# Kernel optimization log

Hardware: AMD Instinct MI355X
Metric: run time of the kernel (lower is better)

Reference implementation:

```python
import jax, jax.numpy as jnp
import numpy as np

T, B, D, H = 256, 128, 512, 512  # seq_len, batch, input_dim, hidden_dim (= n_qubits)


def setup_inputs() -> dict:
    key = jax.random.key(0)
    ks = jax.random.split(key, 17)
    s = 0.02
    inp = {"inputs": jax.random.normal(ks[0], (T, B, D), dtype=jnp.float32)}
    for j, n in enumerate(["f", "i", "u", "o"]):
        inp["W" + n] = jax.random.normal(ks[1 + 4 * j], (D + H, H), dtype=jnp.float32) * s
        inp["b" + n] = jnp.zeros((H,), jnp.float32)
        inp["rx" + n] = jax.random.normal(ks[2 + 4 * j], (H,), dtype=jnp.float32)
        inp["P" + n] = jax.random.normal(ks[3 + 4 * j], (H, H), dtype=jnp.float32) * s
    return inp


def _qlayer(z, rx, P):
    # per-wire trainable rotation RX(theta) acting on the scalar feature of each
    # wire (scales it by cos(theta)), followed by the bias-free `pre` linear.
    return (z * jnp.cos(rx)) @ P


def reference(inputs, Wf, bf, Wi, bi, Wu, bu, Wo, bo, rxf, rxi, rxu, rxo, Pf, Pi, Pu, Po):
    Bc, Hc = inputs.shape[1], bf.shape[0]

    def step(carry, x_t):
        hx, cx = carry
        comb = jnp.concatenate([x_t, hx], axis=1)  # (B, D+H)
        f = jax.nn.sigmoid(_qlayer(comb @ Wf + bf, rxf, Pf))
        i = jax.nn.sigmoid(_qlayer(comb @ Wi + bi, rxi, Pi))
        g = jnp.tanh(_qlayer(comb @ Wu + bu, rxu, Pu))
        o = jax.nn.sigmoid(_qlayer(comb @ Wo + bo, rxo, Po))
        cx = f * cx + i * g
        hx = o * jnp.tanh(cx)
        return (hx, cx), hx

    h0 = jnp.zeros((Bc, Hc), inputs.dtype)
    (hx, cx), outputs = jax.lax.scan(step, (h0, h0), inputs)
    return outputs, hx, cx
```

## Files before the change

### kernel.cpp

```cpp
#include <hip/hip_runtime.h>
#include <hip/hip_bf16.h>

typedef __attribute__((ext_vector_type(8))) short bf16x8;
typedef __attribute__((ext_vector_type(4))) float f32x4;
typedef unsigned short u16;
typedef unsigned int u32;

__device__ __forceinline__ u16 f2bf(float f) {
  union { float f; unsigned u; } v; v.f = f;
  unsigned r = v.u + 0x7FFFu + ((v.u >> 16) & 1u);
  return (u16)(r >> 16);
}

__device__ __forceinline__ float sigm_fast(float x) {
  return __builtin_amdgcn_rcpf(1.f + __expf(-x));
}
__device__ __forceinline__ float tanh_fast(float x) {
  x = fminf(fmaxf(x, -15.f), 15.f);
  float e = __expf(2.f * x);
  return (e - 1.f) * __builtin_amdgcn_rcpf(e + 1.f);
}

__device__ __forceinline__ void ld_llc_b128(const u16* p, bf16x8& r) {
  asm volatile("global_load_dwordx4 %0, %1, off sc0 sc1" : "=&v"(r) : "v"(p));
}
__device__ __forceinline__ void ld_g_b128(const u16* p, bf16x8& r) {
  asm volatile("global_load_dwordx4 %0, %1, off" : "=&v"(r) : "v"(p));
}
__device__ __forceinline__ void st_llc_b32(u32* p, u32 v) {
  asm volatile("global_store_dword %0, %1, off sc0 sc1" :: "v"(p), "v"(v) : "memory");
}
__device__ __forceinline__ void st_g_b32(u32* p, u32 v) {
  asm volatile("global_store_dword %0, %1, off" :: "v"(p), "v"(v) : "memory");
}

__global__ __launch_bounds__(256) void fold_kernel(
    const float* __restrict__ W0, const float* __restrict__ rx0, const float* __restrict__ P0,
    const float* __restrict__ W1, const float* __restrict__ rx1, const float* __restrict__ P1,
    const float* __restrict__ W2, const float* __restrict__ rx2, const float* __restrict__ P2,
    const float* __restrict__ W3, const float* __restrict__ rx3, const float* __restrict__ P3,
    u16* __restrict__ Wt)
{
  const int g = blockIdx.z;
  const float* W  = (g == 0) ? W0  : (g == 1) ? W1  : (g == 2) ? W2  : W3;
  const float* rx = (g == 0) ? rx0 : (g == 1) ? rx1 : (g == 2) ? rx2 : rx3;
  const float* P  = (g == 0) ? P0  : (g == 1) ? P1  : (g == 2) ? P2  : P3;
  __shared__ __align__(16) float As[16][68];
  __shared__ __align__(16) float Bs[16][68];
  const int bk = blockIdx.x, bj = blockIdx.y;
  const int tid = threadIdx.x;
  const int tx = tid & 15, ty = tid >> 4;
  const int j0 = bj * 64, k0 = bk * 64;
  float acc[4][4] = {};
  for (int m0 = 0; m0 < 512; m0 += 16) {
#pragma unroll
    for (int l = 0; l < 4; ++l) {
      int lin = tid + 256 * l;
      int mm = lin >> 6, jr = lin & 63;
      As[mm][jr] = P[(m0 + mm) * 512 + j0 + jr];
      int kk = lin >> 4, mb = lin & 15;
      Bs[mb][kk] = W[(k0 + kk) * 512 + m0 + mb] * cosf(rx[m0 + mb]);
    }
    __syncthreads();
#pragma unroll
    for (int mm = 0; mm < 16; ++mm) {
      f32x4 a = *(const f32x4*)&As[mm][ty * 4];
      f32x4 b = *(const f32x4*)&Bs[mm][tx * 4];
#pragma unroll
      for (int i = 0; i < 4; ++i)
#pragma unroll
        for (int jj = 0; jj < 4; ++jj)
          acc[i][jj] += a[i] * b[jj];
    }
    __syncthreads();
  }
#pragma unroll
  for (int i = 0; i < 4; ++i) {
    int j = j0 + ty * 4 + i;
    size_t n = (size_t)(j * 4 + g);
    ushort4 w;
    w.x = f2bf(acc[i][0]); w.y = f2bf(acc[i][1]);
    w.z = f2bf(acc[i][2]); w.w = f2bf(acc[i][3]);
    *(ushort4*)(Wt + n * 1024 + k0 + tx * 4) = w;
  }
}

__global__ __launch_bounds__(256) void fold_bias(
    const float* __restrict__ b0, const float* __restrict__ rx0, const float* __restrict__ P0,
    const float* __restrict__ b1, const float* __restrict__ rx1, const float* __restrict__ P1,
    const float* __restrict__ b2, const float* __restrict__ rx2, const float* __restrict__ P2,
    const float* __restrict__ b3, const float* __restrict__ rx3, const float* __restrict__ P3,
    float* __restrict__ bpn)
{
  const int g = blockIdx.x >> 3, jb = blockIdx.x & 7;
  const float* b  = (g == 0) ? b0  : (g == 1) ? b1  : (g == 2) ? b2  : b3;
  const float* rx = (g == 0) ? rx0 : (g == 1) ? rx1 : (g == 2) ? rx2 : rx3;
  const float* P  = (g == 0) ? P0  : (g == 1) ? P1  : (g == 2) ? P2  : P3;
  __shared__ float bc[512];
  __shared__ float red[4][65];
  const int tid = threadIdx.x;
  bc[tid] = b[tid] * cosf(rx[tid]);
  bc[tid + 256] = b[tid + 256] * cosf(rx[tid + 256]);
  __syncthreads();
  const int jl = tid & 63, msub = tid >> 6;
  const int j = jb * 64 + jl;
  float acc = 0.f;
  for (int m = msub * 128; m < msub * 128 + 128; ++m)
    acc += bc[m] * P[m * 512 + j];
  red[msub][jl] = acc;
  __syncthreads();
  if (msub == 0)
    bpn[j * 4 + g] = red[0][jl] + red[1][jl] + red[2][jl] + red[3][jl];
}

__global__ __launch_bounds__(256) void xcvt_kernel(
    const float* __restrict__ x, u16* __restrict__ xb)
{
  size_t i = (size_t)blockIdx.x * 256 + threadIdx.x;
  f32x4 v = *(const f32x4*)(x + i * 4);
  ushort4 w;
  w.x = f2bf(v[0]); w.y = f2bf(v[1]); w.z = f2bf(v[2]); w.w = f2bf(v[3]);
  *(ushort4*)(xb + i * 4) = w;
}

__global__ __launch_bounds__(256) void init_kernel(unsigned* hbuf32, float* cbuf,
                                                   unsigned* flags) {
  int i = blockIdx.x * 256 + threadIdx.x;
  hbuf32[i] = 0;
  cbuf[i] = 0.f;
  if (i < 256) flags[i] = 0;
}

__global__ __launch_bounds__(256) void tail_kernel(
    const float* __restrict__ hlast, const float* __restrict__ c,
    float* __restrict__ hx, float* __restrict__ cx)
{
  int i = blockIdx.x * 256 + threadIdx.x;
  hx[i] = hlast[i];
  cx[i] = c[i];
}

__global__ __launch_bounds__(256) void step_kernel(
    const u16* __restrict__ xb_t, const u16* __restrict__ h_in,
    u16* __restrict__ h_out, const u16* __restrict__ Wt,
    const float* __restrict__ bpn, float* __restrict__ cbuf,
    float* __restrict__ out_t)
{
  __shared__ float pre_s[32][33];
  const int bid = blockIdx.x;
  const int mb = bid >> 6, nb = bid & 63;
  const int b0 = mb * 32, n0 = nb * 32;
  const int tid = threadIdx.x;
  const int wv = tid >> 6, lane = tid & 63;
  const int rt = wv >> 1, nt = wv & 1;
  const int l15 = lane & 15, kg = lane >> 4;
  const int brow = b0 + rt * 16 + l15;
  const int ncol = n0 + nt * 16 + l15;
  const u16* wrow = Wt + (size_t)ncol * 1024;
  const u16* xrow = xb_t + (size_t)brow * 512;
  const u16* hrow = h_in + (size_t)brow * 512;
  f32x4 acc = {0.f, 0.f, 0.f, 0.f};
#pragma unroll 8
  for (int kk = 0; kk < 32; ++kk) {
    const int kb = kk * 32 + kg * 8;
    bf16x8 bfrag = *(const bf16x8*)(wrow + kb);
    bf16x8 afrag;
    if (kb < 512) afrag = *(const bf16x8*)(xrow + kb);
    else          afrag = *(const bf16x8*)(hrow + (kb - 512));
    acc = __builtin_amdgcn_mfma_f32_16x16x32_bf16(afrag, bfrag, acc, 0, 0, 0);
  }
  const float bias = bpn[ncol];
#pragma unroll
  for (int q = 0; q < 4; ++q)
    pre_s[rt * 16 + kg * 4 + q][nt * 16 + l15] = acc[q] + bias;
  __syncthreads();
  const int bb = tid >> 3, jo = tid & 7;
  float pf = pre_s[bb][jo * 4 + 0];
  float pi = pre_s[bb][jo * 4 + 1];
  float pu = pre_s[bb][jo * 4 + 2];
  float po = pre_s[bb][jo * 4 + 3];
  float fg = 1.f / (1.f + __expf(-pf));
  float ig = 1.f / (1.f + __expf(-pi));
  float gg = tanhf(pu);
  float og = 1.f / (1.f + __expf(-po));
  size_t idx = (size_t)(b0 + bb) * 512 + (size_t)(nb * 8 + jo);
  float cv = fg * cbuf[idx] + ig * gg;
  cbuf[idx] = cv;
  float hv = og * tanhf(cv);
  out_t[idx] = hv;
  h_out[idx] = f2bf(hv);
}

__global__ __launch_bounds__(256, 1) void qlstm_persistent(
    const u16* __restrict__ Xbf,
    u16* __restrict__ hbuf,
    const u16* __restrict__ Wt,
    const float* __restrict__ bpn,
    float* __restrict__ out,
    unsigned* __restrict__ flags)
{
  __shared__ float pre_s[32][33];
  const int bid = blockIdx.x;
  const int mb = bid >> 6, nb = bid & 63;
  const int b0 = mb * 32, n0 = nb * 32;
  const int tid = threadIdx.x;
  const int wv = tid >> 6, lane = tid & 63;
  const int rt = wv >> 1, nt = wv & 1;
  const int l15 = lane & 15, kg = lane >> 4;
  const int brow = b0 + rt * 16 + l15;
  const int ncol = n0 + nt * 16 + l15;

  const u16* wrow = Wt + (size_t)ncol * 1024;
  bf16x8 warr[32];
#pragma unroll
  for (int kk = 0; kk < 32; ++kk)
    warr[kk] = *(const bf16x8*)(wrow + kk * 32 + kg * 8);
  const float bnc = bpn[ncol];

  const int bb = tid >> 3, jo = tid & 7;
  const size_t eidx = (size_t)(b0 + bb) * 512 + (size_t)(nb * 8 + jo);
  float cst = 0.f, hl = 0.f;

  bf16x8 xf[16];
  {
    const u16* xr = Xbf + (size_t)brow * 512;
#pragma unroll
    for (int kk = 0; kk < 16; ++kk)
      ld_g_b128(xr + kk * 32 + kg * 8, xf[kk]);
    asm volatile("s_waitcnt vmcnt(0)" ::: "memory");
  }

  for (int t = 0; t < 256; ++t) {
    if (t > 0 && tid < 64) {
      int guard = 0;
      while (__hip_atomic_load(&flags[mb * 64 + tid], __ATOMIC_RELAXED,
                               __HIP_MEMORY_SCOPE_AGENT) < (unsigned)t) {
        __builtin_amdgcn_s_sleep(1);
        if (++guard > 8000) break;
      }
    }
    __builtin_amdgcn_s_barrier();
    asm volatile("" ::: "memory");

    bf16x8 hf[16];
    if (t > 0) {
      const u16* hr = hbuf + (size_t)((t & 1) ? 65536 : 0) + (size_t)brow * 512;
#pragma unroll
      for (int kk = 0; kk < 16; ++kk)
        ld_llc_b128(hr + kk * 32 + kg * 8, hf[kk]);
    }

    asm volatile("s_waitcnt vmcnt(16)" ::: "memory");
    __builtin_amdgcn_sched_barrier(0);
    f32x4 ax0 = {0,0,0,0}, ax1 = {0,0,0,0};
#pragma unroll
    for (int kk = 0; kk < 16; kk += 2) {
      ax0 = __builtin_amdgcn_mfma_f32_16x16x32_bf16(xf[kk],     warr[kk],     ax0, 0, 0, 0);
      ax1 = __builtin_amdgcn_mfma_f32_16x16x32_bf16(xf[kk + 1], warr[kk + 1], ax1, 0, 0, 0);
    }

    f32x4 ah0 = {0,0,0,0}, ah1 = {0,0,0,0};
    if (t > 0) {
      asm volatile("s_waitcnt vmcnt(0)" ::: "memory");
      __builtin_amdgcn_sched_barrier(0);
#pragma unroll
      for (int kk = 0; kk < 16; kk += 2) {
        ah0 = __builtin_amdgcn_mfma_f32_16x16x32_bf16(hf[kk],     warr[16 + kk],     ah0, 0, 0, 0);
        ah1 = __builtin_amdgcn_mfma_f32_16x16x32_bf16(hf[kk + 1], warr[16 + kk + 1], ah1, 0, 0, 0);
      }
    }
    f32x4 acc = (ax0 + ax1) + (ah0 + ah1);

#pragma unroll
    for (int q = 0; q < 4; ++q)
      pre_s[rt * 16 + kg * 4 + q][nt * 16 + l15] = acc[q] + bnc;
    asm volatile("s_waitcnt lgkmcnt(0)" ::: "memory");
    __builtin_amdgcn_sched_barrier(0);
    __builtin_amdgcn_s_barrier();
    asm volatile("" ::: "memory");

    float pf = pre_s[bb][jo * 4 + 0];
    float pi = pre_s[bb][jo * 4 + 1];
    float pu = pre_s[bb][jo * 4 + 2];
    float po = pre_s[bb][jo * 4 + 3];
    cst = sigm_fast(pf) * cst + sigm_fast(pi) * tanh_fast(pu);
    float hv = sigm_fast(po) * tanh_fast(cst);
    hl = hv;

    u16 myh = f2bf(hv);
    u32 partner = (u32)(u16)__shfl_xor((int)(u32)myh, 1);
    u16* hnext = hbuf + (size_t)(((t + 1) & 1) ? 65536 : 0);
    if ((tid & 1) == 0)
      st_llc_b32((u32*)(hnext + eidx), (u32)myh | (partner << 16));
    asm volatile("s_waitcnt vmcnt(0)" ::: "memory");
    __builtin_amdgcn_s_barrier();
    asm volatile("" ::: "memory");
    if (tid == 0)
      __hip_atomic_store(&flags[bid], (unsigned)(t + 1), __ATOMIC_RELAXED,
                         __HIP_MEMORY_SCOPE_AGENT);

    union { float f; u32 u; } ho; ho.f = hv;
    st_g_b32((u32*)(out + (size_t)t * 65536 + eidx), ho.u);
    if (t < 255) {
      const u16* xr = Xbf + (size_t)(t + 1) * 65536 + (size_t)brow * 512;
#pragma unroll
      for (int kk = 0; kk < 16; ++kk)
        ld_g_b128(xr + kk * 32 + kg * 8, xf[kk]);
    }
  }

  asm volatile("s_waitcnt vmcnt(0)" ::: "memory");
  out[(size_t)256 * 65536 + eidx] = hl;
  out[(size_t)256 * 65536 + 65536 + eidx] = cst;
}

extern "C" void kernel_launch(void* const* d_in, const int* in_sizes, int n_in,
                              void* d_out, int out_size, void* d_ws, size_t ws_size,
                              hipStream_t stream) {
  (void)in_sizes; (void)n_in; (void)out_size; (void)ws_size;
  const float* inp = (const float*)d_in[0];
  float* out = (float*)d_out;

  char* base = (char*)d_ws;
  u16*      Xbf   = (u16*)base;
  u16*      Wt    = (u16*)(base + 33554432);
  float*    bpn   = (float*)(base + 33554432 + 4194304);
  u16*      hbuf  = (u16*)(base + 33554432 + 4194304 + 8192);
  unsigned* flags = (unsigned*)(base + 33554432 + 4194304 + 8192 + 262144);
  float*    cbuf  = (float*)(base + 33554432 + 4194304 + 8192 + 262144 + 1024);

  const float* W[4];  const float* b[4];  const float* rx[4];  const float* P[4];
  for (int g = 0; g < 4; ++g) {
    W[g]  = (const float*)d_in[1 + 4 * g];
    b[g]  = (const float*)d_in[2 + 4 * g];
    rx[g] = (const float*)d_in[3 + 4 * g];
    P[g]  = (const float*)d_in[4 + 4 * g];
  }
  fold_kernel<<<dim3(16, 8, 4), 256, 0, stream>>>(
      W[0], rx[0], P[0], W[1], rx[1], P[1],
      W[2], rx[2], P[2], W[3], rx[3], P[3], Wt);
  fold_bias<<<dim3(32), 256, 0, stream>>>(
      b[0], rx[0], P[0], b[1], rx[1], P[1],
      b[2], rx[2], P[2], b[3], rx[3], P[3], bpn);
  xcvt_kernel<<<16384, 256, 0, stream>>>(inp, Xbf);
  init_kernel<<<256, 256, 0, stream>>>((unsigned*)hbuf, cbuf, flags);

  void* args[6];
  const u16* Xbf_c = Xbf;
  const u16* Wt_c = Wt;
  const float* bpn_c = bpn;
  u16* hbuf_p = hbuf;
  float* out_p = out;
  unsigned* flags_p = flags;
  args[0] = (void*)&Xbf_c;
  args[1] = (void*)&hbuf_p;
  args[2] = (void*)&Wt_c;
  args[3] = (void*)&bpn_c;
  args[4] = (void*)&out_p;
  args[5] = (void*)&flags_p;
  hipError_t e = hipLaunchCooperativeKernel((const void*)qlstm_persistent,
                                            dim3(256), dim3(256), args, 0, stream);
  if (e != hipSuccess) {
    for (int t = 0; t < 256; ++t) {
      const u16* xb_t  = Xbf + (size_t)t * 65536;
      const u16* h_in  = hbuf + (size_t)(t & 1) * 65536;
      u16*       h_oup = hbuf + (size_t)((t & 1) ^ 1) * 65536;
      float*     out_t = out + (size_t)t * 65536;
      step_kernel<<<256, 256, 0, stream>>>(xb_t, h_in, h_oup, Wt, bpn, cbuf, out_t);
    }
    tail_kernel<<<256, 256, 0, stream>>>(out + (size_t)255 * 65536, cbuf,
                                         out + (size_t)256 * 65536,
                                         out + (size_t)256 * 65536 + 65536);
  }
}
```

Baseline: 1.403 ms.

## Replace flag-based grid sync with sentinel-poisoned h slab polling

Removes the per-step flag array and block barrier wait, and instead makes consumers poll the h data itself. Slots in a 4-deep h ring are poisoned with a NaN sentinel pattern, and loads are retried until no sentinel remains. Each block re-poisons slot t+2 ahead of time. h stores are widened to 128-bit writes by shuffling four packed words into one lane, and pre_s is double-buffered so the trailing barrier can go. Block-to-tile mapping also changes so batch tiles interleave. The scheme relies on bf16 h never equalling the sentinel pair and on store ordering across the ring. It adds retry loads when data is not yet ready.

```diff
diff --git a/kernel.cpp b/kernel.cpp
--- a/kernel.cpp
+++ b/kernel.cpp
@@ -3,8 +3,11 @@
 
 typedef __attribute__((ext_vector_type(8))) short bf16x8;
 typedef __attribute__((ext_vector_type(4))) float f32x4;
+typedef __attribute__((ext_vector_type(4))) unsigned int u32x4;
 typedef unsigned short u16;
 typedef unsigned int u32;
+
+#define SENT 0x7FC07FC0u
 
 __device__ __forceinline__ u16 f2bf(float f) {
   union { float f; unsigned u; } v; v.f = f;
@@ -27,8 +30,8 @@
 __device__ __forceinline__ void ld_g_b128(const u16* p, bf16x8& r) {
   asm volatile("global_load_dwordx4 %0, %1, off" : "=&v"(r) : "v"(p));
 }
-__device__ __forceinline__ void st_llc_b32(u32* p, u32 v) {
-  asm volatile("global_store_dword %0, %1, off sc0 sc1" :: "v"(p), "v"(v) : "memory");
+__device__ __forceinline__ void st_llc_b128(u16* p, u32x4 v) {
+  asm volatile("global_store_dwordx4 %0, %1, off sc0 sc1" :: "v"(p), "v"(v) : "memory");
 }
 __device__ __forceinline__ void st_g_b32(u32* p, u32 v) {
   asm volatile("global_store_dword %0, %1, off" :: "v"(p), "v"(v) : "memory");
@@ -123,12 +126,13 @@
   *(ushort4*)(xb + i * 4) = w;
 }
 
-__global__ __launch_bounds__(256) void init_kernel(unsigned* hbuf32, float* cbuf,
-                                                   unsigned* flags) {
+__global__ __launch_bounds__(256) void init_kernel(u32* hslab32, u32* hz32,
+                                                   float* cbuf) {
   int i = blockIdx.x * 256 + threadIdx.x;
-  hbuf32[i] = 0;
+  hslab32[i] = SENT;
+  hslab32[i + 65536] = SENT;
+  hz32[i] = 0;
   cbuf[i] = 0.f;
-  if (i < 256) flags[i] = 0;
 }
 
 __global__ __launch_bounds__(256) void tail_kernel(
@@ -193,15 +197,14 @@
 
 __global__ __launch_bounds__(256, 1) void qlstm_persistent(
     const u16* __restrict__ Xbf,
-    u16* __restrict__ hbuf,
+    u16* __restrict__ hslab,
     const u16* __restrict__ Wt,
     const float* __restrict__ bpn,
-    float* __restrict__ out,
-    unsigned* __restrict__ flags)
-{
-  __shared__ float pre_s[32][33];
+    float* __restrict__ out)
+{
+  __shared__ float pre_s[2][32][33];
   const int bid = blockIdx.x;
-  const int mb = bid >> 6, nb = bid & 63;
+  const int mb = bid & 3, nb = bid >> 2;
   const int b0 = mb * 32, n0 = nb * 32;
   const int tid = threadIdx.x;
   const int wv = tid >> 6, lane = tid & 63;
@@ -219,6 +222,9 @@
 
   const int bb = tid >> 3, jo = tid & 7;
   const size_t eidx = (size_t)(b0 + bb) * 512 + (size_t)(nb * 8 + jo);
+  const bool pst = ((tid & 7) == 0);
+  const size_t prow_off = (size_t)(b0 + (tid >> 3)) * 512 + (size_t)(nb * 8);
+  const u32x4 sentv = {SENT, SENT, SENT, SENT};
   float cst = 0.f, hl = 0.f;
 
   bf16x8 xf[16];
@@ -231,27 +237,16 @@
   }
 
   for (int t = 0; t < 256; ++t) {
-    if (t > 0 && tid < 64) {
-      int guard = 0;
-      while (__hip_atomic_load(&flags[mb * 64 + tid], __ATOMIC_RELAXED,
-                               __HIP_MEMORY_SCOPE_AGENT) < (unsigned)t) {
-        __builtin_amdgcn_s_sleep(1);
-        if (++guard > 8000) break;
-      }
-    }
-    __builtin_amdgcn_s_barrier();
-    asm volatile("" ::: "memory");
-
+    const u16* hr = hslab + (size_t)(t & 3) * 65536 + (size_t)brow * 512;
     bf16x8 hf[16];
     if (t > 0) {
-      const u16* hr = hbuf + (size_t)((t & 1) ? 65536 : 0) + (size_t)brow * 512;
 #pragma unroll
       for (int kk = 0; kk < 16; ++kk)
         ld_llc_b128(hr + kk * 32 + kg * 8, hf[kk]);
     }
-
     asm volatile("s_waitcnt vmcnt(16)" ::: "memory");
     __builtin_amdgcn_sched_barrier(0);
+
     f32x4 ax0 = {0,0,0,0}, ax1 = {0,0,0,0};
 #pragma unroll
     for (int kk = 0; kk < 16; kk += 2) {
@@ -261,7 +256,24 @@
 
     f32x4 ah0 = {0,0,0,0}, ah1 = {0,0,0,0};
     if (t > 0) {
-      asm volatile("s_waitcnt vmcnt(0)" ::: "memory");
+      int guard = 0;
+      for (;;) {
+        asm volatile("s_waitcnt vmcnt(0)" ::: "memory");
+        __builtin_amdgcn_sched_barrier(0);
+        u32 bad = 0;
+#pragma unroll
+        for (int kk = 0; kk < 16; ++kk) {
+          union { bf16x8 v; u32 d[4]; } u; u.v = hf[kk];
+          bad |= (u.d[0] == SENT) | (u.d[1] == SENT)
+               | (u.d[2] == SENT) | (u.d[3] == SENT);
+        }
+        if (__all((int)(bad == 0))) break;
+        if (++guard > 30000) break;
+        __builtin_amdgcn_s_sleep(1);
+#pragma unroll
+        for (int kk = 0; kk < 16; ++kk)
+          ld_llc_b128(hr + kk * 32 + kg * 8, hf[kk]);
+      }
       __builtin_amdgcn_sched_barrier(0);
 #pragma unroll
       for (int kk = 0; kk < 16; kk += 2) {
@@ -271,34 +283,36 @@
     }
     f32x4 acc = (ax0 + ax1) + (ah0 + ah1);
 
+    if (pst)
+      st_llc_b128(hslab + (size_t)((t + 2) & 3) * 65536 + prow_off, sentv);
+
 #pragma unroll
     for (int q = 0; q < 4; ++q)
-      pre_s[rt * 16 + kg * 4 + q][nt * 16 + l15] = acc[q] + bnc;
+      pre_s[t & 1][rt * 16 + kg * 4 + q][nt * 16 + l15] = acc[q] + bnc;
     asm volatile("s_waitcnt lgkmcnt(0)" ::: "memory");
     __builtin_amdgcn_sched_barrier(0);
     __builtin_amdgcn_s_barrier();
     asm volatile("" ::: "memory");
 
-    float pf = pre_s[bb][jo * 4 + 0];
-    float pi = pre_s[bb][jo * 4 + 1];
-    float pu = pre_s[bb][jo * 4 + 2];
-    float po = pre_s[bb][jo * 4 + 3];
+    float pf = pre_s[t & 1][bb][jo * 4 + 0];
+    float pi = pre_s[t & 1][bb][jo * 4 + 1];
+    float pu = pre_s[t & 1][bb][jo * 4 + 2];
+    float po = pre_s[t & 1][bb][jo * 4 + 3];
     cst = sigm_fast(pf) * cst + sigm_fast(pi) * tanh_fast(pu);
     float hv = sigm_fast(po) * tanh_fast(cst);
     hl = hv;
 
     u16 myh = f2bf(hv);
-    u32 partner = (u32)(u16)__shfl_xor((int)(u32)myh, 1);
-    u16* hnext = hbuf + (size_t)(((t + 1) & 1) ? 65536 : 0);
-    if ((tid & 1) == 0)
-      st_llc_b32((u32*)(hnext + eidx), (u32)myh | (partner << 16));
+    u32 w  = (u32)myh | ((u32)(u16)__shfl_xor((int)(u32)myh, 1) << 16);
+    u32 d1 = (u32)__shfl_xor((int)w, 2);
+    u32 d2 = (u32)__shfl_xor((int)w, 4);
+    u32 d3 = (u32)__shfl_xor((int)w, 6);
+
     asm volatile("s_waitcnt vmcnt(0)" ::: "memory");
-    __builtin_amdgcn_s_barrier();
-    asm volatile("" ::: "memory");
-    if (tid == 0)
-      __hip_atomic_store(&flags[bid], (unsigned)(t + 1), __ATOMIC_RELAXED,
-                         __HIP_MEMORY_SCOPE_AGENT);
-
+    if (pst) {
+      u32x4 hw = {w, d1, d2, d3};
+      st_llc_b128(hslab + (size_t)((t + 1) & 3) * 65536 + prow_off, hw);
+    }
     union { float f; u32 u; } ho; ho.f = hv;
     st_g_b32((u32*)(out + (size_t)t * 65536 + eidx), ho.u);
     if (t < 255) {
@@ -322,12 +336,12 @@
   float* out = (float*)d_out;
 
   char* base = (char*)d_ws;
-  u16*      Xbf   = (u16*)base;
-  u16*      Wt    = (u16*)(base + 33554432);
-  float*    bpn   = (float*)(base + 33554432 + 4194304);
-  u16*      hbuf  = (u16*)(base + 33554432 + 4194304 + 8192);
-  unsigned* flags = (unsigned*)(base + 33554432 + 4194304 + 8192 + 262144);
-  float*    cbuf  = (float*)(base + 33554432 + 4194304 + 8192 + 262144 + 1024);
+  u16*   Xbf   = (u16*)base;
+  u16*   Wt    = (u16*)(base + 33554432);
+  float* bpn   = (float*)(base + 33554432 + 4194304);
+  u16*   hslab = (u16*)(base + 33554432 + 4194304 + 8192);
+  u16*   hz    = (u16*)(base + 33554432 + 4194304 + 8192 + 524288);
+  float* cbuf  = (float*)(base + 33554432 + 4194304 + 8192 + 524288 + 262144);
 
   const float* W[4];  const float* b[4];  const float* rx[4];  const float* P[4];
   for (int g = 0; g < 4; ++g) {
@@ -343,28 +357,26 @@
       b[0], rx[0], P[0], b[1], rx[1], P[1],
       b[2], rx[2], P[2], b[3], rx[3], P[3], bpn);
   xcvt_kernel<<<16384, 256, 0, stream>>>(inp, Xbf);
-  init_kernel<<<256, 256, 0, stream>>>((unsigned*)hbuf, cbuf, flags);
-
-  void* args[6];
+  init_kernel<<<256, 256, 0, stream>>>((u32*)hslab, (u32*)hz, cbuf);
+
+  void* args[5];
   const u16* Xbf_c = Xbf;
   const u16* Wt_c = Wt;
   const float* bpn_c = bpn;
-  u16* hbuf_p = hbuf;
+  u16* hslab_p = hslab;
   float* out_p = out;
-  unsigned* flags_p = flags;
   args[0] = (void*)&Xbf_c;
-  args[1] = (void*)&hbuf_p;
+  args[1] = (void*)&hslab_p;
   args[2] = (void*)&Wt_c;
   args[3] = (void*)&bpn_c;
   args[4] = (void*)&out_p;
-  args[5] = (void*)&flags_p;
   hipError_t e = hipLaunchCooperativeKernel((const void*)qlstm_persistent,
                                             dim3(256), dim3(256), args, 0, stream);
   if (e != hipSuccess) {
     for (int t = 0; t < 256; ++t) {
       const u16* xb_t  = Xbf + (size_t)t * 65536;
-      const u16* h_in  = hbuf + (size_t)(t & 1) * 65536;
-      u16*       h_oup = hbuf + (size_t)((t & 1) ^ 1) * 65536;
+      const u16* h_in  = hz + (size_t)(t & 1) * 65536;
+      u16*       h_oup = hz + (size_t)((t & 1) ^ 1) * 65536;
       float*     out_t = out + (size_t)t * 65536;
       step_kernel<<<256, 256, 0, stream>>>(xb_t, h_in, h_oup, Wt, bpn, cbuf, out_t);
     }
```

New measurement: 1.660 ms. 1.18x slower.

## Restructure persistent LSTM into 128 blocks of 512 threads with LDS-staged h

Applied to the files above, without the earlier changes.

The persistent recurrent kernel now runs 128 workgroups of 512 threads, each owning 32 batch rows by 64 gate columns, instead of 256 workgroups of 256 threads. Each step the block loads its 32 rows of the bf16 hidden state from global memory cooperatively once, stores them to a swizzled LDS tile, and every wave reads its MFMA operands from LDS. Per-wave redundant global loads go away, and the flag wait covers 32 producers instead of 64. Hidden-state stores are packed into 64-bit writes. The trade-off is an extra LDS round trip and barrier per step, higher register pressure at 512 threads, and fewer blocks doing the serial per-step work.

```diff
diff --git a/kernel.cpp b/kernel.cpp
--- a/kernel.cpp
+++ b/kernel.cpp
@@ -3,6 +3,7 @@
 
 typedef __attribute__((ext_vector_type(8))) short bf16x8;
 typedef __attribute__((ext_vector_type(4))) float f32x4;
+typedef __attribute__((ext_vector_type(2))) unsigned int u32x2;
 typedef unsigned short u16;
 typedef unsigned int u32;
 
@@ -27,8 +28,8 @@
 __device__ __forceinline__ void ld_g_b128(const u16* p, bf16x8& r) {
   asm volatile("global_load_dwordx4 %0, %1, off" : "=&v"(r) : "v"(p));
 }
-__device__ __forceinline__ void st_llc_b32(u32* p, u32 v) {
-  asm volatile("global_store_dword %0, %1, off sc0 sc1" :: "v"(p), "v"(v) : "memory");
+__device__ __forceinline__ void st_llc_b64(u16* p, u32x2 v) {
+  asm volatile("global_store_dwordx2 %0, %1, off sc0 sc1" :: "v"(p), "v"(v) : "memory");
 }
 __device__ __forceinline__ void st_g_b32(u32* p, u32 v) {
   asm volatile("global_store_dword %0, %1, off" :: "v"(p), "v"(v) : "memory");
@@ -123,12 +124,12 @@
   *(ushort4*)(xb + i * 4) = w;
 }
 
-__global__ __launch_bounds__(256) void init_kernel(unsigned* hbuf32, float* cbuf,
-                                                   unsigned* flags) {
+__global__ __launch_bounds__(256) void init_kernel(u32* hbuf32, float* cbuf,
+                                                   u32* flags) {
   int i = blockIdx.x * 256 + threadIdx.x;
   hbuf32[i] = 0;
   cbuf[i] = 0.f;
-  if (i < 256) flags[i] = 0;
+  if (i < 128) flags[i] = 0;
 }
 
 __global__ __launch_bounds__(256) void tail_kernel(
@@ -191,24 +192,27 @@
   h_out[idx] = f2bf(hv);
 }
 
-__global__ __launch_bounds__(256, 1) void qlstm_persistent(
+__global__ __launch_bounds__(512, 2) void qlstm_persistent(
     const u16* __restrict__ Xbf,
     u16* __restrict__ hbuf,
     const u16* __restrict__ Wt,
     const float* __restrict__ bpn,
     float* __restrict__ out,
-    unsigned* __restrict__ flags)
-{
-  __shared__ float pre_s[32][33];
+    u32* __restrict__ flags)
+{
+  __shared__ __align__(16) u16 hs[16384];
+  __shared__ float pre_s[32][68];
   const int bid = blockIdx.x;
-  const int mb = bid >> 6, nb = bid & 63;
-  const int b0 = mb * 32, n0 = nb * 32;
+  const int mb = bid & 3, nb = bid >> 2;
+  const int b0 = mb * 32;
   const int tid = threadIdx.x;
   const int wv = tid >> 6, lane = tid & 63;
-  const int rt = wv >> 1, nt = wv & 1;
+  const int rt = wv >> 2;
+  const int ct = wv & 3;
   const int l15 = lane & 15, kg = lane >> 4;
   const int brow = b0 + rt * 16 + l15;
-  const int ncol = n0 + nt * 16 + l15;
+  const int rloc = rt * 16 + l15;
+  const int ncol = nb * 64 + ct * 16 + l15;
 
   const u16* wrow = Wt + (size_t)ncol * 1024;
   bf16x8 warr[32];
@@ -217,8 +221,8 @@
     warr[kk] = *(const bf16x8*)(wrow + kk * 32 + kg * 8);
   const float bnc = bpn[ncol];
 
-  const int bb = tid >> 3, jo = tid & 7;
-  const size_t eidx = (size_t)(b0 + bb) * 512 + (size_t)(nb * 8 + jo);
+  const int crow = tid >> 4, jl = tid & 15;
+  const size_t eidx = (size_t)(b0 + crow) * 512 + (size_t)(nb * 16 + jl);
   float cst = 0.f, hl = 0.f;
 
   bf16x8 xf[16];
@@ -227,30 +231,29 @@
 #pragma unroll
     for (int kk = 0; kk < 16; ++kk)
       ld_g_b128(xr + kk * 32 + kg * 8, xf[kk]);
-    asm volatile("s_waitcnt vmcnt(0)" ::: "memory");
   }
 
   for (int t = 0; t < 256; ++t) {
-    if (t > 0 && tid < 64) {
+    if (t > 0 && tid < 32) {
       int guard = 0;
-      while (__hip_atomic_load(&flags[mb * 64 + tid], __ATOMIC_RELAXED,
-                               __HIP_MEMORY_SCOPE_AGENT) < (unsigned)t) {
+      while (__hip_atomic_load(&flags[mb + 4 * tid], __ATOMIC_RELAXED,
+                               __HIP_MEMORY_SCOPE_AGENT) < (u32)t) {
         __builtin_amdgcn_s_sleep(1);
-        if (++guard > 8000) break;
+        if (++guard > 30000) break;
       }
     }
     __builtin_amdgcn_s_barrier();
     asm volatile("" ::: "memory");
 
-    bf16x8 hf[16];
-    if (t > 0) {
-      const u16* hr = hbuf + (size_t)((t & 1) ? 65536 : 0) + (size_t)brow * 512;
-#pragma unroll
-      for (int kk = 0; kk < 16; ++kk)
-        ld_llc_b128(hr + kk * 32 + kg * 8, hf[kk]);
-    }
-
-    asm volatile("s_waitcnt vmcnt(16)" ::: "memory");
+    bf16x8 sv[4];
+    {
+      const u16* hg = hbuf + (size_t)((t & 1) ? 65536 : 0) + (size_t)b0 * 512;
+#pragma unroll
+      for (int r = 0; r < 4; ++r)
+        ld_llc_b128(hg + ((size_t)(r * 512 + tid) * 16) / 2, sv[r]);
+    }
+
+    asm volatile("s_waitcnt vmcnt(4)" ::: "memory");
     __builtin_amdgcn_sched_barrier(0);
     f32x4 ax0 = {0,0,0,0}, ax1 = {0,0,0,0};
 #pragma unroll
@@ -259,44 +262,62 @@
       ax1 = __builtin_amdgcn_mfma_f32_16x16x32_bf16(xf[kk + 1], warr[kk + 1], ax1, 0, 0, 0);
     }
 
-    f32x4 ah0 = {0,0,0,0}, ah1 = {0,0,0,0};
-    if (t > 0) {
-      asm volatile("s_waitcnt vmcnt(0)" ::: "memory");
-      __builtin_amdgcn_sched_barrier(0);
-#pragma unroll
-      for (int kk = 0; kk < 16; kk += 2) {
-        ah0 = __builtin_amdgcn_mfma_f32_16x16x32_bf16(hf[kk],     warr[16 + kk],     ah0, 0, 0, 0);
-        ah1 = __builtin_amdgcn_mfma_f32_16x16x32_bf16(hf[kk + 1], warr[16 + kk + 1], ah1, 0, 0, 0);
-      }
-    }
-    f32x4 acc = (ax0 + ax1) + (ah0 + ah1);
-
-#pragma unroll
-    for (int q = 0; q < 4; ++q)
-      pre_s[rt * 16 + kg * 4 + q][nt * 16 + l15] = acc[q] + bnc;
+    asm volatile("s_waitcnt vmcnt(0)" ::: "memory");
+    __builtin_amdgcn_sched_barrier(0);
+#pragma unroll
+    for (int r = 0; r < 4; ++r) {
+      int o = (r * 512 + tid) * 16;
+      int row = o >> 10, cb = o & 1023;
+      *(bf16x8*)((char*)hs + row * 1024 + (cb ^ ((row & 7) << 4))) = sv[r];
+    }
     asm volatile("s_waitcnt lgkmcnt(0)" ::: "memory");
     __builtin_amdgcn_sched_barrier(0);
     __builtin_amdgcn_s_barrier();
     asm volatile("" ::: "memory");
 
-    float pf = pre_s[bb][jo * 4 + 0];
-    float pi = pre_s[bb][jo * 4 + 1];
-    float pu = pre_s[bb][jo * 4 + 2];
-    float po = pre_s[bb][jo * 4 + 3];
+    f32x4 ah0 = {0,0,0,0}, ah1 = {0,0,0,0};
+#pragma unroll
+    for (int kk = 0; kk < 16; kk += 2) {
+      int cb0 = (kk * 32 + kg * 8) * 2;
+      int cb1 = ((kk + 1) * 32 + kg * 8) * 2;
+      bf16x8 h0 = *(const bf16x8*)((const char*)hs + rloc * 1024 +
+                                   (cb0 ^ ((rloc & 7) << 4)));
+      bf16x8 h1 = *(const bf16x8*)((const char*)hs + rloc * 1024 +
+                                   (cb1 ^ ((rloc & 7) << 4)));
+      ah0 = __builtin_amdgcn_mfma_f32_16x16x32_bf16(h0, warr[16 + kk],     ah0, 0, 0, 0);
+      ah1 = __builtin_amdgcn_mfma_f32_16x16x32_bf16(h1, warr[16 + kk + 1], ah1, 0, 0, 0);
+    }
+    f32x4 acc = (ax0 + ax1) + (ah0 + ah1);
+
+#pragma unroll
+    for (int q = 0; q < 4; ++q)
+      pre_s[rt * 16 + kg * 4 + q][ct * 16 + l15] = acc[q] + bnc;
+    asm volatile("s_waitcnt lgkmcnt(0)" ::: "memory");
+    __builtin_amdgcn_sched_barrier(0);
+    __builtin_amdgcn_s_barrier();
+    asm volatile("" ::: "memory");
+
+    float pf = pre_s[crow][jl * 4 + 0];
+    float pi = pre_s[crow][jl * 4 + 1];
+    float pu = pre_s[crow][jl * 4 + 2];
+    float po = pre_s[crow][jl * 4 + 3];
     cst = sigm_fast(pf) * cst + sigm_fast(pi) * tanh_fast(pu);
     float hv = sigm_fast(po) * tanh_fast(cst);
     hl = hv;
 
     u16 myh = f2bf(hv);
-    u32 partner = (u32)(u16)__shfl_xor((int)(u32)myh, 1);
+    u32 w  = (u32)myh | ((u32)(u16)__shfl_xor((int)(u32)myh, 1) << 16);
+    u32 w2 = (u32)__shfl_xor((int)w, 2);
     u16* hnext = hbuf + (size_t)(((t + 1) & 1) ? 65536 : 0);
-    if ((tid & 1) == 0)
-      st_llc_b32((u32*)(hnext + eidx), (u32)myh | (partner << 16));
+    if ((tid & 3) == 0) {
+      u32x2 hw = {w, w2};
+      st_llc_b64(hnext + (size_t)(b0 + crow) * 512 + (size_t)(nb * 16 + jl), hw);
+    }
     asm volatile("s_waitcnt vmcnt(0)" ::: "memory");
     __builtin_amdgcn_s_barrier();
     asm volatile("" ::: "memory");
     if (tid == 0)
-      __hip_atomic_store(&flags[bid], (unsigned)(t + 1), __ATOMIC_RELAXED,
+      __hip_atomic_store(&flags[bid], (u32)(t + 1), __ATOMIC_RELAXED,
                          __HIP_MEMORY_SCOPE_AGENT);
 
     union { float f; u32 u; } ho; ho.f = hv;
@@ -322,12 +343,12 @@
   float* out = (float*)d_out;
 
   char* base = (char*)d_ws;
-  u16*      Xbf   = (u16*)base;
-  u16*      Wt    = (u16*)(base + 33554432);
-  float*    bpn   = (float*)(base + 33554432 + 4194304);
-  u16*      hbuf  = (u16*)(base + 33554432 + 4194304 + 8192);
-  unsigned* flags = (unsigned*)(base + 33554432 + 4194304 + 8192 + 262144);
-  float*    cbuf  = (float*)(base + 33554432 + 4194304 + 8192 + 262144 + 1024);
+  u16*   Xbf   = (u16*)base;
+  u16*   Wt    = (u16*)(base + 33554432);
+  float* bpn   = (float*)(base + 33554432 + 4194304);
+  u16*   hbuf  = (u16*)(base + 33554432 + 4194304 + 8192);
+  u32*   flags = (u32*)(base + 33554432 + 4194304 + 8192 + 262144);
+  float* cbuf  = (float*)(base + 33554432 + 4194304 + 8192 + 262144 + 1024);
 
   const float* W[4];  const float* b[4];  const float* rx[4];  const float* P[4];
   for (int g = 0; g < 4; ++g) {
@@ -343,7 +364,7 @@
       b[0], rx[0], P[0], b[1], rx[1], P[1],
       b[2], rx[2], P[2], b[3], rx[3], P[3], bpn);
   xcvt_kernel<<<16384, 256, 0, stream>>>(inp, Xbf);
-  init_kernel<<<256, 256, 0, stream>>>((unsigned*)hbuf, cbuf, flags);
+  init_kernel<<<256, 256, 0, stream>>>((u32*)hbuf, cbuf, flags);
 
   void* args[6];
   const u16* Xbf_c = Xbf;
@@ -351,7 +372,7 @@
   const float* bpn_c = bpn;
   u16* hbuf_p = hbuf;
   float* out_p = out;
-  unsigned* flags_p = flags;
+  u32* flags_p = flags;
   args[0] = (void*)&Xbf_c;
   args[1] = (void*)&hbuf_p;
   args[2] = (void*)&Wt_c;
@@ -359,7 +380,7 @@
   args[4] = (void*)&out_p;
   args[5] = (void*)&flags_p;
   hipError_t e = hipLaunchCooperativeKernel((const void*)qlstm_persistent,
-                                            dim3(256), dim3(256), args, 0, stream);
+                                            dim3(128), dim3(512), args, 0, stream);
   if (e != hipSuccess) {
     for (int t = 0; t < 256; ++t) {
       const u16* xb_t  = Xbf + (size_t)t * 65536;
```

After: 1.631 ms. 1.16x slower.
